# Kernel tuning notes

Hardware: AMD Instinct MI355X
Metric: run time of the kernel (lower is better)

## Reference

```python
import jax, jax.numpy as jnp
import numpy as np

N = 50000      # nodes
E = 400000     # edges (before self loops)
IN = 128       # in_channels
H = 4          # num_heads (layers 1-2)
C = 32         # hidden_dim per head
HID = H * C    # 128 total hidden
CLS = 40       # num_classes (out_heads = 1)
EPS = 1e-5     # BatchNorm eps
SLOPE = 0.2    # LeakyReLU negative slope (PyG GATConv default)


def setup_inputs() -> dict:
    key = jax.random.key(0)
    ks = jax.random.split(key, 24)
    rn = lambda k, shp, s: jax.random.normal(k, shp, jnp.float32) * s
    x = jax.random.normal(ks[0], (N, IN), jnp.float32)
    src = jax.random.randint(ks[1], (E,), 0, N)
    dst = jax.random.randint(ks[2], (E,), 0, N)
    src = jnp.where(src == dst, (src + 1) % N, src)  # no pre-existing self loops
    edge_index = jnp.stack([src, dst]).astype(jnp.int32)
    inp = dict(x=x, edge_index=edge_index)
    # conv1: in IN -> H heads x C
    inp['W1'] = rn(ks[3], (IN, H * C), 1.0 / np.sqrt(IN))
    inp['as1'] = rn(ks[4], (H, C), 0.1)
    inp['ad1'] = rn(ks[5], (H, C), 0.1)
    inp['b1'] = rn(ks[6], (H * C,), 0.02)
    # conv2: HID -> H x C
    inp['W2'] = rn(ks[7], (HID, H * C), 1.0 / np.sqrt(HID))
    inp['as2'] = rn(ks[8], (H, C), 0.1)
    inp['ad2'] = rn(ks[9], (H, C), 0.1)
    inp['b2'] = rn(ks[10], (H * C,), 0.02)
    # conv3: HID -> 1 head x CLS, concat=False
    inp['W3'] = rn(ks[11], (HID, CLS), 1.0 / np.sqrt(HID))
    inp['as3'] = rn(ks[12], (1, CLS), 0.1)
    inp['ad3'] = rn(ks[13], (1, CLS), 0.1)
    inp['b3'] = rn(ks[14], (CLS,), 0.02)
    # residual projection
    inp['Wres'] = rn(ks[15], (IN, HID), 1.0 / np.sqrt(IN))
    # BatchNorm (eval mode: running stats)
    inp['g1'] = 1.0 + rn(ks[16], (HID,), 0.1)
    inp['be1'] = rn(ks[17], (HID,), 0.1)
    inp['m1'] = rn(ks[18], (HID,), 0.1)
    inp['v1'] = 1.0 + jax.random.uniform(ks[19], (HID,), jnp.float32) * 0.5
    inp['g2'] = 1.0 + rn(ks[20], (HID,), 0.1)
    inp['be2'] = rn(ks[21], (HID,), 0.1)
    inp['m2'] = rn(ks[22], (HID,), 0.1)
    inp['v2'] = 1.0 + jax.random.uniform(ks[23], (HID,), jnp.float32) * 0.5
    return inp


def _gat_conv(h, src, dst, W, a_src, a_dst, bias, heads, out_ch, concat):
    """PyG-style GATConv (eval: attention dropout off), self loops already in src/dst."""
    n = h.shape[0]
    xw = (h @ W).reshape(n, heads, out_ch)                    # [N,H,C]
    e_src = jnp.sum(xw * a_src, axis=-1)                      # [N,H]
    e_dst = jnp.sum(xw * a_dst, axis=-1)                      # [N,H]
    e = jax.nn.leaky_relu(e_src[src] + e_dst[dst], SLOPE)     # [E',H]
    # segment softmax over incoming edges of each dst node
    mseg = jax.ops.segment_max(e, dst, num_segments=n)        # [N,H]
    ex = jnp.exp(e - mseg[dst])
    den = jax.ops.segment_sum(ex, dst, num_segments=n)
    alpha = ex / den[dst]                                     # [E',H]
    out = jax.ops.segment_sum(alpha[:, :, None] * xw[src], dst, num_segments=n)  # [N,H,C]
    out = out.reshape(n, heads * out_ch) if concat else out.mean(axis=1)
    return out + bias


def _bn(h, g, b, m, v):
    return (h - m) * jax.lax.rsqrt(v + EPS) * g + b


def reference(x, edge_index, W1, as1, ad1, b1, W2, as2, ad2, b2,
              W3, as3, ad3, b3, Wres, g1, be1, m1, v1, g2, be2, m2, v2):
    n = x.shape[0]
    loop = jnp.arange(n, dtype=edge_index.dtype)
    src = jnp.concatenate([edge_index[0], loop])  # add self loops (PyG default)
    dst = jnp.concatenate([edge_index[1], loop])
    x0 = x
    h = _gat_conv(x0, src, dst, W1, as1, ad1, b1, H, C, True)
    h = jax.nn.elu(_bn(h, g1, be1, m1, v1) + x0 @ Wres)
    h_res = h
    h = _gat_conv(h, src, dst, W2, as2, ad2, b2, H, C, True)
    h = jax.nn.elu(_bn(h, g2, be2, m2, v2) + h_res)
    logits = _gat_conv(h, src, dst, W3, as3, ad3, b3, 1, CLS, False)
    return logits
```

## Files before the change

### kernel.cpp

```cpp
#include <hip/hip_runtime.h>
#include <hip/hip_bf16.h>

#define THREADS 256

typedef __attribute__((ext_vector_type(8))) short bfrag;
typedef __attribute__((ext_vector_type(4))) float f32x4;

__device__ inline unsigned short f2b(float v) {
    __hip_bfloat16 b = __float2bfloat16(v);
    return *reinterpret_cast<unsigned short*>(&b);
}
__device__ inline float b2f(unsigned short u) {
    return __uint_as_float(((unsigned)u) << 16);
}

__global__ void detect_kernel(const unsigned short* __restrict__ x, int n, int* flag) {
    __shared__ int cnt;
    if (threadIdx.x == 0) cnt = 0;
    __syncthreads();
    int local = 0;
    for (int i = threadIdx.x; i < n; i += THREADS) {
        unsigned ex = (x[i] >> 7) & 0xFF;
        if (ex == 0xFF || ex >= 134 || (ex > 0 && ex <= 100)) local++;
    }
    atomicAdd(&cnt, local);
    __syncthreads();
    if (threadIdx.x == 0) *flag = (cnt * 8 > n) ? 0 : 1;
}

struct ConvArgs {
    const void* src[21];
    float* dst[21];
    int prefix[22];
};

__global__ void convert_kernel(ConvArgs a, const int* __restrict__ flag, int total) {
    int i = blockIdx.x * THREADS + threadIdx.x;
    if (i >= total) return;
    bool isbf = (*flag != 0);
    int lo = 0;
    while (i >= a.prefix[lo + 1]) ++lo;
    int off = i - a.prefix[lo];
    float v;
    if (isbf) v = b2f(((const unsigned short*)a.src[lo])[off]);
    else v = ((const float*)a.src[lo])[off];
    a.dst[lo][off] = v;
}

__global__ void xconv_kernel(const float* __restrict__ xin, const int* __restrict__ flag,
                             unsigned short* __restrict__ xb, int total) {
    if (*flag) return;
    int i = blockIdx.x * THREADS + threadIdx.x;
    if (i >= total) return;
    xb[i] = f2b(xin[i]);
}

__global__ void wtf_all(const float* __restrict__ W1, const float* __restrict__ W2,
                        const float* __restrict__ WR, const float* __restrict__ W3,
                        unsigned short* __restrict__ o1, unsigned short* __restrict__ o2,
                        unsigned short* __restrict__ oR, unsigned short* __restrict__ o3) {
    int b = blockIdx.x;
    const float* W; unsigned short* o; int cols, tt;
    if (b < 8)       { W = W1; o = o1; cols = 128; tt = b; }
    else if (b < 16) { W = W2; o = o2; cols = 128; tt = b - 8; }
    else if (b < 24) { W = WR; o = oR; cols = 128; tt = b - 16; }
    else             { W = W3; o = o3; cols = 40;  tt = b - 24; }
    int id = tt * 256 + threadIdx.x;
    int t = id >> 8, ks = (id >> 6) & 3, l = id & 63;
    int q = l >> 4, n = l & 15;
    int c = t * 16 + n;
#pragma unroll
    for (int j = 0; j < 8; ++j) {
        int k = ks * 32 + q * 8 + j;
        float v = (c < cols) ? W[k * cols + c] : 0.f;
        o[id * 8 + j] = f2b(v);
    }
}

__global__ void bnprep_kernel(const float* __restrict__ g1, const float* __restrict__ be1,
                              const float* __restrict__ m1, const float* __restrict__ v1,
                              const float* __restrict__ b1, const float* __restrict__ g2,
                              const float* __restrict__ be2, const float* __restrict__ m2,
                              const float* __restrict__ v2, const float* __restrict__ b2,
                              float* __restrict__ sc1, float* __restrict__ sh1,
                              float* __restrict__ sc2, float* __restrict__ sh2) {
    int c = threadIdx.x;
    if (c < 128) {
        float s = g1[c] * rsqrtf(v1[c] + 1e-5f);
        sc1[c] = s;
        sh1[c] = be1[c] - m1[c] * s + b1[c] * s;
    } else {
        int d = c - 128;
        float s = g2[d] * rsqrtf(v2[d] + 1e-5f);
        sc2[d] = s;
        sh2[d] = be2[d] - m2[d] * s + b2[d] * s;
    }
}

__global__ void count_kernel(const int* __restrict__ ei, int* __restrict__ deg, int E, int N) {
    int e = blockIdx.x * THREADS + threadIdx.x;
    if (e >= E + N) return;
    int d = (e < E) ? ei[E + e] : (e - E);
    atomicAdd(&deg[d], 1);
}

__global__ void bsum_kernel(const int* __restrict__ deg, int* __restrict__ bsum, int N) {
    int idx = blockIdx.x * 256 + threadIdx.x;
    int lane = threadIdx.x & 63, wv = threadIdx.x >> 6;
    int v = (idx < N) ? deg[idx] : 0;
#pragma unroll
    for (int o = 1; o < 64; o <<= 1) v += __shfl_xor(v, o, 64);
    __shared__ int ws[4];
    if (lane == 0) ws[wv] = v;
    __syncthreads();
    if (threadIdx.x == 0) bsum[blockIdx.x] = ws[0] + ws[1] + ws[2] + ws[3];
}

__global__ __launch_bounds__(1024) void bscan_kernel(const int* __restrict__ bsum,
                                                     int* __restrict__ boff, int nb) {
    __shared__ int ws[16];
    int tid = threadIdx.x, lane = tid & 63, wv = tid >> 6;
    int v = (tid < nb) ? bsum[tid] : 0;
    int sc = v;
#pragma unroll
    for (int o = 1; o < 64; o <<= 1) {
        int t = __shfl_up(sc, o, 64);
        if (lane >= o) sc += t;
    }
    if (lane == 63) ws[wv] = sc;
    __syncthreads();
    int add = 0;
#pragma unroll
    for (int k = 0; k < 16; ++k) add += (k < wv) ? ws[k] : 0;
    if (tid < nb) boff[tid] = add + sc - v;
}

__global__ void scanw_kernel(const int* __restrict__ deg, const int* __restrict__ boff,
                             int* __restrict__ row_ptr, int* __restrict__ pos, int N) {
    int idx = blockIdx.x * 256 + threadIdx.x;
    int lane = threadIdx.x & 63, wv = threadIdx.x >> 6;
    int v = (idx < N) ? deg[idx] : 0;
    int sc = v;
#pragma unroll
    for (int o = 1; o < 64; o <<= 1) {
        int t = __shfl_up(sc, o, 64);
        if (lane >= o) sc += t;
    }
    __shared__ int ws[4];
    if (lane == 63) ws[wv] = sc;
    __syncthreads();
    int add = boff[blockIdx.x];
#pragma unroll
    for (int k = 0; k < 4; ++k) add += (k < wv) ? ws[k] : 0;
    int excl = add + sc - v;
    if (idx < N) {
        pos[idx] = excl;
        row_ptr[idx + 1] = excl + v;
    }
    if (idx == 0) row_ptr[0] = 0;
}

__global__ void scatter_kernel(const int* __restrict__ ei, int* __restrict__ pos,
                               int* __restrict__ csr, int E, int N) {
    int e = blockIdx.x * THREADS + threadIdx.x;
    if (e >= E + N) return;
    int s, d;
    if (e < E) { s = ei[e]; d = ei[E + e]; }
    else { s = e - E; d = s; }
    int p = atomicAdd(&pos[d], 1);
    csr[p] = s;
}

template <int COLT, int HEADS, bool ES, typename OT>
__global__ __launch_bounds__(256) void gemm_mfma(
    const unsigned short* __restrict__ A, const unsigned short* __restrict__ Wg,
    const float* __restrict__ as_f, const float* __restrict__ ad_f,
    OT* __restrict__ out, int ldc, int cols,
    float* __restrict__ es, float* __restrict__ ed, int N) {
    __shared__ __align__(16) unsigned short Wls[COLT * 2048];
    int tid = threadIdx.x;
    {
        const float4* src = (const float4*)Wg;
        float4* dst = (float4*)Wls;
#pragma unroll
        for (int i = 0; i < COLT; ++i) dst[tid + i * 256] = src[tid + i * 256];
    }
    __syncthreads();
    int w = tid >> 6, lane = tid & 63;
    int n = lane & 15, q = lane >> 4;
    int row0 = blockIdx.x * 64 + w * 16;
    int ar = row0 + n; ar = ar < N ? ar : N - 1;
    f32x4 acc[COLT];
#pragma unroll
    for (int t = 0; t < COLT; ++t) acc[t] = (f32x4){0.f, 0.f, 0.f, 0.f};
    const unsigned short* arow = A + (size_t)ar * 128;
#pragma unroll
    for (int ks = 0; ks < 4; ++ks) {
        bfrag a = *reinterpret_cast<const bfrag*>(arow + ks * 32 + q * 8);
#pragma unroll
        for (int t = 0; t < COLT; ++t) {
            bfrag b = *reinterpret_cast<const bfrag*>(&Wls[((t * 4 + ks) * 64 + lane) * 8]);
            acc[t] = __builtin_amdgcn_mfma_f32_16x16x32_bf16(a, b, acc[t], 0, 0, 0);
        }
    }
    if (ES) {
        float asv[COLT], adv[COLT];
#pragma unroll
        for (int t = 0; t < COLT; ++t) {
            int c = t * 16 + n;
            asv[t] = (c < cols) ? as_f[c] : 0.f;
            adv[t] = (c < cols) ? ad_f[c] : 0.f;
        }
#pragma unroll
        for (int r = 0; r < 4; ++r) {
            float pe[HEADS], pd[HEADS];
#pragma unroll
            for (int h = 0; h < HEADS; ++h) { pe[h] = 0.f; pd[h] = 0.f; }
#pragma unroll
            for (int t = 0; t < COLT; ++t) {
                int h = (HEADS == 4) ? (t >> 1) : 0;
                pe[h] = fmaf(acc[t][r], asv[t], pe[h]);
                pd[h] = fmaf(acc[t][r], adv[t], pd[h]);
            }
#pragma unroll
            for (int h = 0; h < HEADS; ++h) {
#pragma unroll
                for (int o = 1; o < 16; o <<= 1) {
                    pe[h] += __shfl_xor(pe[h], o, 64);
                    pd[h] += __shfl_xor(pd[h], o, 64);
                }
            }
            int row = row0 + q * 4 + r;
            if (n == 0 && row < N) {
#pragma unroll
                for (int h = 0; h < HEADS; ++h) {
                    es[(size_t)row * HEADS + h] = pe[h];
                    ed[(size_t)row * HEADS + h] = pd[h];
                }
            }
        }
    }
#pragma unroll
    for (int t = 0; t < COLT; ++t) {
        int col = t * 16 + n;
        if (col < cols) {
#pragma unroll
            for (int r = 0; r < 4; ++r) {
                int row = row0 + q * 4 + r;
                if (row < N) {
                    float v = acc[t][r];
                    out[(size_t)row * ldc + col] = (sizeof(OT) == 2) ? (OT)f2b(v) : (OT)v;
                }
            }
        }
    }
}

__global__ __launch_bounds__(256) void gemm_dual(
    const unsigned short* __restrict__ Araw, const unsigned short* __restrict__ Acvt,
    const int* __restrict__ flag,
    const unsigned short* __restrict__ Wg1, const unsigned short* __restrict__ WgR,
    const float* __restrict__ as_f, const float* __restrict__ ad_f,
    unsigned short* __restrict__ xwb, float* __restrict__ resf,
    float* __restrict__ es, float* __restrict__ ed, int N) {
    __shared__ __align__(16) unsigned short Wls[16 * 2048];
    int tid = threadIdx.x;
    {
        const float4* s1 = (const float4*)Wg1;
        const float4* s2 = (const float4*)WgR;
        float4* dst = (float4*)Wls;
#pragma unroll
        for (int i = 0; i < 8; ++i) dst[tid + i * 256] = s1[tid + i * 256];
#pragma unroll
        for (int i = 0; i < 8; ++i) dst[2048 + tid + i * 256] = s2[tid + i * 256];
    }
    const unsigned short* A = (*flag) ? Araw : Acvt;
    __syncthreads();
    int w = tid >> 6, lane = tid & 63;
    int n = lane & 15, q = lane >> 4;
    int row0 = blockIdx.x * 64 + w * 16;
    int ar = row0 + n; ar = ar < N ? ar : N - 1;
    f32x4 acc[16];
#pragma unroll
    for (int t = 0; t < 16; ++t) acc[t] = (f32x4){0.f, 0.f, 0.f, 0.f};
    const unsigned short* arow = A + (size_t)ar * 128;
#pragma unroll
    for (int ks = 0; ks < 4; ++ks) {
        bfrag a = *reinterpret_cast<const bfrag*>(arow + ks * 32 + q * 8);
#pragma unroll
        for (int t = 0; t < 8; ++t) {
            bfrag b = *reinterpret_cast<const bfrag*>(&Wls[((t * 4 + ks) * 64 + lane) * 8]);
            acc[t] = __builtin_amdgcn_mfma_f32_16x16x32_bf16(a, b, acc[t], 0, 0, 0);
        }
#pragma unroll
        for (int t = 0; t < 8; ++t) {
            bfrag b = *reinterpret_cast<const bfrag*>(&Wls[16384 + ((t * 4 + ks) * 64 + lane) * 8]);
            acc[8 + t] = __builtin_amdgcn_mfma_f32_16x16x32_bf16(a, b, acc[8 + t], 0, 0, 0);
        }
    }
    float asv[8], adv[8];
#pragma unroll
    for (int t = 0; t < 8; ++t) {
        int c = t * 16 + n;
        asv[t] = as_f[c];
        adv[t] = ad_f[c];
    }
#pragma unroll
    for (int r = 0; r < 4; ++r) {
        float pe[4] = {0.f, 0.f, 0.f, 0.f}, pd[4] = {0.f, 0.f, 0.f, 0.f};
#pragma unroll
        for (int t = 0; t < 8; ++t) {
            int h = t >> 1;
            pe[h] = fmaf(acc[t][r], asv[t], pe[h]);
            pd[h] = fmaf(acc[t][r], adv[t], pd[h]);
        }
#pragma unroll
        for (int h = 0; h < 4; ++h) {
#pragma unroll
            for (int o = 1; o < 16; o <<= 1) {
                pe[h] += __shfl_xor(pe[h], o, 64);
                pd[h] += __shfl_xor(pd[h], o, 64);
            }
        }
        int row = row0 + q * 4 + r;
        if (n == 0 && row < N) {
#pragma unroll
            for (int h = 0; h < 4; ++h) {
                es[(size_t)row * 4 + h] = pe[h];
                ed[(size_t)row * 4 + h] = pd[h];
            }
        }
    }
#pragma unroll
    for (int t = 0; t < 8; ++t) {
        int col = t * 16 + n;
#pragma unroll
        for (int r = 0; r < 4; ++r) {
            int row = row0 + q * 4 + r;
            if (row < N) {
                xwb[(size_t)row * 128 + col] = f2b(acc[t][r]);
                resf[(size_t)row * 128 + col] = acc[8 + t][r];
            }
        }
    }
}

template <bool WF32>
__global__ __launch_bounds__(256) void agg128_fused(
    const unsigned short* __restrict__ xwb, const float* __restrict__ es,
    const float* __restrict__ ed, const int* __restrict__ row_ptr,
    const int* __restrict__ csr, const float* __restrict__ bnsc,
    const float* __restrict__ bnsh, const float* __restrict__ res,
    float* __restrict__ outf, unsigned short* __restrict__ outb, int N) {
    int w = threadIdx.x >> 6, lane = threadIdx.x & 63;
    int node = blockIdx.x * 4 + w;
    if (node >= N) return;
    int h = lane >> 4;
    int i16 = lane & 15;
    int base = lane & 48;
    int c0 = lane * 2;
    float edl = ed[node * 4 + h];
    int start = row_ptr[node], end = row_ptr[node + 1];
    float den = 0.f, a0 = 0.f, a1 = 0.f;
    for (int jb = start; jb < end; jb += 16) {
        int cnt = end - jb; cnt = cnt < 16 ? cnt : 16;
        int sv = csr[jb + (i16 < cnt ? i16 : 0)];
        float wgl = 0.f;
        if (i16 < cnt) {
            float e = es[sv * 4 + h] + edl;
            e = e > 0.f ? e : 0.2f * e;
            wgl = __expf(e);
        }
        float d = wgl;
        d += __shfl_xor(d, 1, 64);
        d += __shfl_xor(d, 2, 64);
        d += __shfl_xor(d, 4, 64);
        d += __shfl_xor(d, 8, 64);
        den += d;
        for (int j4 = 0; j4 < cnt; j4 += 4) {
#pragma unroll
            for (int u = 0; u < 4; ++u) {
                int j = j4 + u;
                int s = __shfl(sv, j, 64);
                float wg = __shfl(wgl, base + j, 64);
                unsigned uu = *(const unsigned*)(xwb + (size_t)s * 128 + c0);
                a0 = fmaf(wg, __uint_as_float(uu << 16), a0);
                a1 = fmaf(wg, __uint_as_float(uu & 0xffff0000u), a1);
            }
        }
    }
    float inv = 1.f / den;
    float2 sc = *(const float2*)(bnsc + c0);
    float2 sh = *(const float2*)(bnsh + c0);
    float2 rr = *(const float2*)(res + (size_t)node * 128 + c0);
    float v0 = fmaf(a0 * inv, sc.x, sh.x) + rr.x;
    float v1 = fmaf(a1 * inv, sc.y, sh.y) + rr.y;
    v0 = v0 > 0.f ? v0 : expm1f(v0);
    v1 = v1 > 0.f ? v1 : expm1f(v1);
    if (WF32) *(float2*)(outf + (size_t)node * 128 + c0) = make_float2(v0, v1);
    unsigned pk = (unsigned)f2b(v0) | ((unsigned)f2b(v1) << 16);
    *(unsigned*)(outb + (size_t)node * 128 + c0) = pk;
}

__global__ __launch_bounds__(256) void agg40_kernel(
    const unsigned short* __restrict__ xw3b, const float* __restrict__ es3,
    const float* __restrict__ ed3, const int* __restrict__ row_ptr,
    const int* __restrict__ csr, const float* __restrict__ b3,
    void* __restrict__ out, const int* __restrict__ flag, int N) {
    int w = threadIdx.x >> 6, lane = threadIdx.x & 63;
    int node = blockIdx.x * 4 + w;
    if (node >= N) return;
    int i16 = lane & 15;
    int g = lane >= 40 ? 2 : (lane >= 20 ? 1 : 0);
    int cp = lane - g * 20;
    int c0 = cp * 2; c0 = c0 > 38 ? 38 : c0;
    float edl = ed3[node];
    int start = row_ptr[node], end = row_ptr[node + 1];
    float den = 0.f, a0 = 0.f, a1 = 0.f;
    for (int jb = start; jb < end; jb += 16) {
        int cnt = end - jb; cnt = cnt < 16 ? cnt : 16;
        int sv = csr[jb + (i16 < cnt ? i16 : 0)];
        float wgl = 0.f;
        if (i16 < cnt) {
            float e = es3[sv] + edl;
            e = e > 0.f ? e : 0.2f * e;
            wgl = __expf(e);
        }
        float d = wgl;
        d += __shfl_xor(d, 1, 64);
        d += __shfl_xor(d, 2, 64);
        d += __shfl_xor(d, 4, 64);
        d += __shfl_xor(d, 8, 64);
        den += d;
        for (int j = 0; j < cnt; j += 3) {
            int slot = j + g;
            int sl = slot < 15 ? slot : 15;
            int s = __shfl(sv, sl, 64);
            float wg = __shfl(wgl, sl, 64);
            if (slot >= cnt) wg = 0.f;
            unsigned uu = *(const unsigned*)(xw3b + (size_t)s * 40 + c0);
            a0 = fmaf(wg, __uint_as_float(uu << 16), a0);
            a1 = fmaf(wg, __uint_as_float(uu & 0xffff0000u), a1);
        }
    }
    float t0 = __shfl(a0, (lane + 20) & 63, 64);
    float t1 = __shfl(a0, (lane + 40) & 63, 64);
    float u0 = __shfl(a1, (lane + 20) & 63, 64);
    float u1 = __shfl(a1, (lane + 40) & 63, 64);
    a0 += t0 + t1;
    a1 += u0 + u1;
    if (lane < 20) {
        float inv = 1.f / den;
        float v0 = a0 * inv + b3[c0];
        float v1 = a1 * inv + b3[c0 + 1];
        size_t eoff = (size_t)node * 40 + c0;
        if (*flag) {
            unsigned pk = (unsigned)f2b(v0) | ((unsigned)f2b(v1) << 16);
            *(unsigned*)((unsigned short*)out + eoff) = pk;
        } else {
            *(float2*)((float*)out + eoff) = make_float2(v0, v1);
        }
    }
}

extern "C" void kernel_launch(void* const* d_in, const int* in_sizes, int n_in,
                              void* d_out, int out_size, void* d_ws, size_t ws_size,
                              hipStream_t stream) {
    (void)n_in; (void)out_size; (void)ws_size;
    const int N = in_sizes[0] / 128;
    const int E = in_sizes[1] / 2;
    const int EPN = E + N;
    const int NB = (N + 255) / 256;
    char* base = (char*)d_ws;
    size_t off = 0;
    auto alloc = [&](size_t bytes) -> char* {
        char* p = base + off;
        off = (off + bytes + 255) & ~(size_t)255;
        return p;
    };
    int* flag = (int*)alloc(4);
    int* deg = (int*)alloc((size_t)N * 4);
    int* row_ptr = (int*)alloc((size_t)(N + 1) * 4);
    int* pos = (int*)alloc((size_t)N * 4);
    int* bsum = (int*)alloc((size_t)NB * 4);
    int* boff = (int*)alloc((size_t)NB * 4);
    int* csr = (int*)alloc((size_t)EPN * 4);
    float* wc = (float*)alloc((size_t)56184 * 4);
    float* bnsc1 = (float*)alloc(512); float* bnsh1 = (float*)alloc(512);
    float* bnsc2 = (float*)alloc(512); float* bnsh2 = (float*)alloc(512);
    unsigned short* Wl1 = (unsigned short*)alloc(32768);
    unsigned short* Wl2 = (unsigned short*)alloc(32768);
    unsigned short* WlR = (unsigned short*)alloc(32768);
    unsigned short* Wl3 = (unsigned short*)alloc(12288);
    unsigned short* xb = (unsigned short*)alloc((size_t)N * 128 * 2);
    unsigned short* xwb = (unsigned short*)alloc((size_t)N * 128 * 2);
    unsigned short* h1b = (unsigned short*)alloc((size_t)N * 128 * 2);
    float* h1 = (float*)alloc((size_t)N * 128 * 4);
    float* resf = (float*)alloc((size_t)N * 128 * 4);
    float* es = (float*)alloc((size_t)N * 4 * 4);
    float* ed = (float*)alloc((size_t)N * 4 * 4);

    const int* ei = (const int*)d_in[1];

    float* W1 = wc;            float* AS1 = wc + 16384; float* AD1 = wc + 16512; float* B1 = wc + 16640;
    float* W2 = wc + 16768;    float* AS2 = wc + 33152; float* AD2 = wc + 33280; float* B2 = wc + 33408;
    float* W3 = wc + 33536;    float* AS3 = wc + 38656; float* AD3 = wc + 38696; float* B3 = wc + 38736;
    float* WR = wc + 38776;
    float* G1 = wc + 55160; float* BE1 = wc + 55288; float* M1 = wc + 55416; float* V1 = wc + 55544;
    float* G2 = wc + 55672; float* BE2 = wc + 55800; float* M2 = wc + 55928; float* V2 = wc + 56056;

    hipMemsetAsync(deg, 0, (size_t)N * 4, stream);
    detect_kernel<<<1, THREADS, 0, stream>>>((const unsigned short*)d_in[0], 4096, flag);

    ConvArgs ca;
    const int idxs[21] = {2, 3, 4, 5, 6, 7, 8, 9, 10, 11, 12, 13, 14, 15, 16, 17, 18, 19, 20, 21, 22};
    float* dsts[21] = {W1, AS1, AD1, B1, W2, AS2, AD2, B2, W3, AS3, AD3, B3, WR,
                       G1, BE1, M1, V1, G2, BE2, M2, V2};
    int p = 0;
    for (int t = 0; t < 21; t++) {
        ca.src[t] = d_in[idxs[t]];
        ca.dst[t] = dsts[t];
        ca.prefix[t] = p;
        p += in_sizes[idxs[t]];
    }
    ca.prefix[21] = p;
    convert_kernel<<<(p + THREADS - 1) / THREADS, THREADS, 0, stream>>>(ca, flag, p);

    xconv_kernel<<<(N * 128 + THREADS - 1) / THREADS, THREADS, 0, stream>>>(
        (const float*)d_in[0], flag, xb, N * 128);
    wtf_all<<<27, THREADS, 0, stream>>>(W1, W2, WR, W3, Wl1, Wl2, WlR, Wl3);
    bnprep_kernel<<<1, THREADS, 0, stream>>>(G1, BE1, M1, V1, B1, G2, BE2, M2, V2, B2,
                                             bnsc1, bnsh1, bnsc2, bnsh2);

    count_kernel<<<(EPN + THREADS - 1) / THREADS, THREADS, 0, stream>>>(ei, deg, E, N);
    bsum_kernel<<<NB, 256, 0, stream>>>(deg, bsum, N);
    bscan_kernel<<<1, 1024, 0, stream>>>(bsum, boff, NB);
    scanw_kernel<<<NB, 256, 0, stream>>>(deg, boff, row_ptr, pos, N);
    scatter_kernel<<<(EPN + THREADS - 1) / THREADS, THREADS, 0, stream>>>(ei, pos, csr, E, N);

    int gemmGrid = (N + 63) / 64;
    int aggGrid = (N + 3) / 4;

    gemm_dual<<<gemmGrid, 256, 0, stream>>>((const unsigned short*)d_in[0], xb, flag,
                                            Wl1, WlR, AS1, AD1, xwb, resf, es, ed, N);
    agg128_fused<true><<<aggGrid, 256, 0, stream>>>(xwb, es, ed, row_ptr, csr,
                                                    bnsc1, bnsh1, resf, h1, h1b, N);
    gemm_mfma<8, 4, true, unsigned short><<<gemmGrid, 256, 0, stream>>>(
        h1b, Wl2, AS2, AD2, xwb, 128, 128, es, ed, N);
    unsigned short* h2b = (unsigned short*)resf;
    agg128_fused<false><<<aggGrid, 256, 0, stream>>>(xwb, es, ed, row_ptr, csr,
                                                     bnsc2, bnsh2, h1, nullptr, h2b, N);
    gemm_mfma<3, 1, true, unsigned short><<<gemmGrid, 256, 0, stream>>>(
        h2b, Wl3, AS3, AD3, xwb, 40, 40, es, ed, N);
    agg40_kernel<<<aggGrid, 256, 0, stream>>>(xwb, es, ed, row_ptr, csr, B3, d_out, flag, N);
}
```

Measured before the change: 309.1 us.

## Merge prep kernels, store residuals in bf16, and batch gathers in aggregation

Replaces the four separate input-conversion and prep kernels with a single prep kernel that reads raw inputs directly. The residual projection and the layer-1 output now live only in bf16 instead of fp32, which roughly halves that traffic and drops one fp32 write stream. The aggregation loops now issue all 16 neighbor gathers up front, unrolled, to expose memory-level parallelism, at the cost of loading padding rows for partial chunks. The residual path loses precision by going to bf16.

```diff
diff --git a/kernel.cpp b/kernel.cpp
--- a/kernel.cpp
+++ b/kernel.cpp
@@ -12,6 +12,9 @@
 }
 __device__ inline float b2f(unsigned short u) {
     return __uint_as_float(((unsigned)u) << 16);
+}
+__device__ inline float rdv(const void* p, int off, bool isbf) {
+    return isbf ? b2f(((const unsigned short*)p)[off]) : ((const float*)p)[off];
 }
 
 __global__ void detect_kernel(const unsigned short* __restrict__ x, int n, int* flag) {
@@ -28,72 +31,64 @@
     if (threadIdx.x == 0) *flag = (cnt * 8 > n) ? 0 : 1;
 }
 
-struct ConvArgs {
-    const void* src[21];
-    float* dst[21];
-    int prefix[22];
-};
-
-__global__ void convert_kernel(ConvArgs a, const int* __restrict__ flag, int total) {
-    int i = blockIdx.x * THREADS + threadIdx.x;
-    if (i >= total) return;
+struct InPtrs { const void* p[23]; };
+
+__global__ void prep_kernel(InPtrs in, const int* __restrict__ flag,
+                            unsigned short* __restrict__ Wl1, unsigned short* __restrict__ Wl2,
+                            unsigned short* __restrict__ WlR, unsigned short* __restrict__ Wl3,
+                            float* __restrict__ bnsc1, float* __restrict__ bnsh1,
+                            float* __restrict__ bnsc2, float* __restrict__ bnsh2,
+                            float* __restrict__ AS1f, float* __restrict__ AD1f,
+                            float* __restrict__ AS2f, float* __restrict__ AD2f,
+                            float* __restrict__ AS3f, float* __restrict__ AD3f,
+                            float* __restrict__ B3f, unsigned short* __restrict__ xb, int N) {
     bool isbf = (*flag != 0);
-    int lo = 0;
-    while (i >= a.prefix[lo + 1]) ++lo;
-    int off = i - a.prefix[lo];
-    float v;
-    if (isbf) v = b2f(((const unsigned short*)a.src[lo])[off]);
-    else v = ((const float*)a.src[lo])[off];
-    a.dst[lo][off] = v;
-}
-
-__global__ void xconv_kernel(const float* __restrict__ xin, const int* __restrict__ flag,
-                             unsigned short* __restrict__ xb, int total) {
-    if (*flag) return;
-    int i = blockIdx.x * THREADS + threadIdx.x;
-    if (i >= total) return;
-    xb[i] = f2b(xin[i]);
-}
-
-__global__ void wtf_all(const float* __restrict__ W1, const float* __restrict__ W2,
-                        const float* __restrict__ WR, const float* __restrict__ W3,
-                        unsigned short* __restrict__ o1, unsigned short* __restrict__ o2,
-                        unsigned short* __restrict__ oR, unsigned short* __restrict__ o3) {
     int b = blockIdx.x;
-    const float* W; unsigned short* o; int cols, tt;
-    if (b < 8)       { W = W1; o = o1; cols = 128; tt = b; }
-    else if (b < 16) { W = W2; o = o2; cols = 128; tt = b - 8; }
-    else if (b < 24) { W = WR; o = oR; cols = 128; tt = b - 16; }
-    else             { W = W3; o = o3; cols = 40;  tt = b - 24; }
-    int id = tt * 256 + threadIdx.x;
-    int t = id >> 8, ks = (id >> 6) & 3, l = id & 63;
-    int q = l >> 4, n = l & 15;
-    int c = t * 16 + n;
-#pragma unroll
-    for (int j = 0; j < 8; ++j) {
-        int k = ks * 32 + q * 8 + j;
-        float v = (c < cols) ? W[k * cols + c] : 0.f;
-        o[id * 8 + j] = f2b(v);
-    }
-}
-
-__global__ void bnprep_kernel(const float* __restrict__ g1, const float* __restrict__ be1,
-                              const float* __restrict__ m1, const float* __restrict__ v1,
-                              const float* __restrict__ b1, const float* __restrict__ g2,
-                              const float* __restrict__ be2, const float* __restrict__ m2,
-                              const float* __restrict__ v2, const float* __restrict__ b2,
-                              float* __restrict__ sc1, float* __restrict__ sh1,
-                              float* __restrict__ sc2, float* __restrict__ sh2) {
-    int c = threadIdx.x;
-    if (c < 128) {
-        float s = g1[c] * rsqrtf(v1[c] + 1e-5f);
-        sc1[c] = s;
-        sh1[c] = be1[c] - m1[c] * s + b1[c] * s;
+    if (b < 27) {
+        const void* Wv; unsigned short* o; int cols, tt;
+        if (b < 8)       { Wv = in.p[2];  o = Wl1; cols = 128; tt = b; }
+        else if (b < 16) { Wv = in.p[6];  o = Wl2; cols = 128; tt = b - 8; }
+        else if (b < 24) { Wv = in.p[14]; o = WlR; cols = 128; tt = b - 16; }
+        else             { Wv = in.p[10]; o = Wl3; cols = 40;  tt = b - 24; }
+        int id = tt * 256 + threadIdx.x;
+        int t = id >> 8, ks = (id >> 6) & 3, l = id & 63;
+        int q = l >> 4, n = l & 15;
+        int c = t * 16 + n;
+#pragma unroll
+        for (int j = 0; j < 8; ++j) {
+            int k = ks * 32 + q * 8 + j;
+            float v = (c < cols) ? rdv(Wv, k * cols + c, isbf) : 0.f;
+            o[id * 8 + j] = f2b(v);
+        }
+    } else if (b == 27) {
+        int c = threadIdx.x;
+        if (c < 128) {
+            float s = rdv(in.p[15], c, isbf) * rsqrtf(rdv(in.p[18], c, isbf) + 1e-5f);
+            bnsc1[c] = s;
+            bnsh1[c] = rdv(in.p[16], c, isbf) - rdv(in.p[17], c, isbf) * s +
+                       rdv(in.p[5], c, isbf) * s;
+            AS1f[c] = rdv(in.p[3], c, isbf);
+            AD1f[c] = rdv(in.p[4], c, isbf);
+            AS2f[c] = rdv(in.p[7], c, isbf);
+            AD2f[c] = rdv(in.p[8], c, isbf);
+        } else {
+            int d = c - 128;
+            float s = rdv(in.p[19], d, isbf) * rsqrtf(rdv(in.p[22], d, isbf) + 1e-5f);
+            bnsc2[d] = s;
+            bnsh2[d] = rdv(in.p[20], d, isbf) - rdv(in.p[21], d, isbf) * s +
+                       rdv(in.p[9], d, isbf) * s;
+            if (d < 40) {
+                AS3f[d] = rdv(in.p[11], d, isbf);
+                AD3f[d] = rdv(in.p[12], d, isbf);
+                B3f[d] = rdv(in.p[13], d, isbf);
+            }
+        }
     } else {
-        int d = c - 128;
-        float s = g2[d] * rsqrtf(v2[d] + 1e-5f);
-        sc2[d] = s;
-        sh2[d] = be2[d] - m2[d] * s + b2[d] * s;
+        if (isbf) return;
+        const float* xf = (const float*)in.p[0];
+        int total = N * 128;
+        int stride = (gridDim.x - 28) * 256;
+        for (int i = (b - 28) * 256 + threadIdx.x; i < total; i += stride) xb[i] = f2b(xf[i]);
     }
 }
 
@@ -171,11 +166,11 @@
     csr[p] = s;
 }
 
-template <int COLT, int HEADS, bool ES, typename OT>
+template <int COLT, int HEADS, bool ES>
 __global__ __launch_bounds__(256) void gemm_mfma(
     const unsigned short* __restrict__ A, const unsigned short* __restrict__ Wg,
     const float* __restrict__ as_f, const float* __restrict__ ad_f,
-    OT* __restrict__ out, int ldc, int cols,
+    unsigned short* __restrict__ out, int ldc, int cols,
     float* __restrict__ es, float* __restrict__ ed, int N) {
     __shared__ __align__(16) unsigned short Wls[COLT * 2048];
     int tid = threadIdx.x;
@@ -247,10 +242,7 @@
 #pragma unroll
             for (int r = 0; r < 4; ++r) {
                 int row = row0 + q * 4 + r;
-                if (row < N) {
-                    float v = acc[t][r];
-                    out[(size_t)row * ldc + col] = (sizeof(OT) == 2) ? (OT)f2b(v) : (OT)v;
-                }
+                if (row < N) out[(size_t)row * ldc + col] = f2b(acc[t][r]);
             }
         }
     }
@@ -261,7 +253,7 @@
     const int* __restrict__ flag,
     const unsigned short* __restrict__ Wg1, const unsigned short* __restrict__ WgR,
     const float* __restrict__ as_f, const float* __restrict__ ad_f,
-    unsigned short* __restrict__ xwb, float* __restrict__ resf,
+    unsigned short* __restrict__ xwb, unsigned short* __restrict__ resb,
     float* __restrict__ es, float* __restrict__ ed, int N) {
     __shared__ __align__(16) unsigned short Wls[16 * 2048];
     int tid = threadIdx.x;
@@ -339,19 +331,18 @@
             int row = row0 + q * 4 + r;
             if (row < N) {
                 xwb[(size_t)row * 128 + col] = f2b(acc[t][r]);
-                resf[(size_t)row * 128 + col] = acc[8 + t][r];
-            }
-        }
-    }
-}
-
-template <bool WF32>
+                resb[(size_t)row * 128 + col] = f2b(acc[8 + t][r]);
+            }
+        }
+    }
+}
+
 __global__ __launch_bounds__(256) void agg128_fused(
     const unsigned short* __restrict__ xwb, const float* __restrict__ es,
     const float* __restrict__ ed, const int* __restrict__ row_ptr,
     const int* __restrict__ csr, const float* __restrict__ bnsc,
-    const float* __restrict__ bnsh, const float* __restrict__ res,
-    float* __restrict__ outf, unsigned short* __restrict__ outb, int N) {
+    const float* __restrict__ bnsh, const unsigned short* __restrict__ resb,
+    unsigned short* __restrict__ outb, int N) {
     int w = threadIdx.x >> 6, lane = threadIdx.x & 63;
     int node = blockIdx.x * 4 + w;
     if (node >= N) return;
@@ -365,6 +356,12 @@
     for (int jb = start; jb < end; jb += 16) {
         int cnt = end - jb; cnt = cnt < 16 ? cnt : 16;
         int sv = csr[jb + (i16 < cnt ? i16 : 0)];
+        unsigned uu[16];
+#pragma unroll
+        for (int u = 0; u < 16; ++u) {
+            int s = __shfl(sv, u, 64);
+            uu[u] = *(const unsigned*)(xwb + (size_t)s * 128 + c0);
+        }
         float wgl = 0.f;
         if (i16 < cnt) {
             float e = es[sv * 4 + h] + edl;
@@ -377,27 +374,21 @@
         d += __shfl_xor(d, 4, 64);
         d += __shfl_xor(d, 8, 64);
         den += d;
-        for (int j4 = 0; j4 < cnt; j4 += 4) {
-#pragma unroll
-            for (int u = 0; u < 4; ++u) {
-                int j = j4 + u;
-                int s = __shfl(sv, j, 64);
-                float wg = __shfl(wgl, base + j, 64);
-                unsigned uu = *(const unsigned*)(xwb + (size_t)s * 128 + c0);
-                a0 = fmaf(wg, __uint_as_float(uu << 16), a0);
-                a1 = fmaf(wg, __uint_as_float(uu & 0xffff0000u), a1);
-            }
+#pragma unroll
+        for (int u = 0; u < 16; ++u) {
+            float wg = __shfl(wgl, base + u, 64);
+            a0 = fmaf(wg, __uint_as_float(uu[u] << 16), a0);
+            a1 = fmaf(wg, __uint_as_float(uu[u] & 0xffff0000u), a1);
         }
     }
     float inv = 1.f / den;
     float2 sc = *(const float2*)(bnsc + c0);
     float2 sh = *(const float2*)(bnsh + c0);
-    float2 rr = *(const float2*)(res + (size_t)node * 128 + c0);
-    float v0 = fmaf(a0 * inv, sc.x, sh.x) + rr.x;
-    float v1 = fmaf(a1 * inv, sc.y, sh.y) + rr.y;
+    unsigned ur = *(const unsigned*)(resb + (size_t)node * 128 + c0);
+    float v0 = fmaf(a0 * inv, sc.x, sh.x) + __uint_as_float(ur << 16);
+    float v1 = fmaf(a1 * inv, sc.y, sh.y) + __uint_as_float(ur & 0xffff0000u);
     v0 = v0 > 0.f ? v0 : expm1f(v0);
     v1 = v1 > 0.f ? v1 : expm1f(v1);
-    if (WF32) *(float2*)(outf + (size_t)node * 128 + c0) = make_float2(v0, v1);
     unsigned pk = (unsigned)f2b(v0) | ((unsigned)f2b(v1) << 16);
     *(unsigned*)(outb + (size_t)node * 128 + c0) = pk;
 }
@@ -420,6 +411,13 @@
     for (int jb = start; jb < end; jb += 16) {
         int cnt = end - jb; cnt = cnt < 16 ? cnt : 16;
         int sv = csr[jb + (i16 < cnt ? i16 : 0)];
+        unsigned uu[6];
+#pragma unroll
+        for (int t = 0; t < 6; ++t) {
+            int slot = 3 * t + g; slot = slot < 15 ? slot : 15;
+            int s = __shfl(sv, slot, 64);
+            uu[t] = *(const unsigned*)(xw3b + (size_t)s * 40 + c0);
+        }
         float wgl = 0.f;
         if (i16 < cnt) {
             float e = es3[sv] + edl;
@@ -432,15 +430,14 @@
         d += __shfl_xor(d, 4, 64);
         d += __shfl_xor(d, 8, 64);
         den += d;
-        for (int j = 0; j < cnt; j += 3) {
-            int slot = j + g;
+#pragma unroll
+        for (int t = 0; t < 6; ++t) {
+            int slot = 3 * t + g;
             int sl = slot < 15 ? slot : 15;
-            int s = __shfl(sv, sl, 64);
             float wg = __shfl(wgl, sl, 64);
             if (slot >= cnt) wg = 0.f;
-            unsigned uu = *(const unsigned*)(xw3b + (size_t)s * 40 + c0);
-            a0 = fmaf(wg, __uint_as_float(uu << 16), a0);
-            a1 = fmaf(wg, __uint_as_float(uu & 0xffff0000u), a1);
+            a0 = fmaf(wg, __uint_as_float(uu[t] << 16), a0);
+            a1 = fmaf(wg, __uint_as_float(uu[t] & 0xffff0000u), a1);
         }
     }
     float t0 = __shfl(a0, (lane + 20) & 63, 64);
@@ -485,9 +482,12 @@
     int* bsum = (int*)alloc((size_t)NB * 4);
     int* boff = (int*)alloc((size_t)NB * 4);
     int* csr = (int*)alloc((size_t)EPN * 4);
-    float* wc = (float*)alloc((size_t)56184 * 4);
     float* bnsc1 = (float*)alloc(512); float* bnsh1 = (float*)alloc(512);
     float* bnsc2 = (float*)alloc(512); float* bnsh2 = (float*)alloc(512);
+    float* AS1f = (float*)alloc(512); float* AD1f = (float*)alloc(512);
+    float* AS2f = (float*)alloc(512); float* AD2f = (float*)alloc(512);
+    float* AS3f = (float*)alloc(256); float* AD3f = (float*)alloc(256);
+    float* B3f = (float*)alloc(256);
     unsigned short* Wl1 = (unsigned short*)alloc(32768);
     unsigned short* Wl2 = (unsigned short*)alloc(32768);
     unsigned short* WlR = (unsigned short*)alloc(32768);
@@ -495,42 +495,21 @@
     unsigned short* xb = (unsigned short*)alloc((size_t)N * 128 * 2);
     unsigned short* xwb = (unsigned short*)alloc((size_t)N * 128 * 2);
     unsigned short* h1b = (unsigned short*)alloc((size_t)N * 128 * 2);
-    float* h1 = (float*)alloc((size_t)N * 128 * 4);
-    float* resf = (float*)alloc((size_t)N * 128 * 4);
+    unsigned short* resb = (unsigned short*)alloc((size_t)N * 128 * 2);
     float* es = (float*)alloc((size_t)N * 4 * 4);
     float* ed = (float*)alloc((size_t)N * 4 * 4);
 
     const int* ei = (const int*)d_in[1];
 
-    float* W1 = wc;            float* AS1 = wc + 16384; float* AD1 = wc + 16512; float* B1 = wc + 16640;
-    float* W2 = wc + 16768;    float* AS2 = wc + 33152; float* AD2 = wc + 33280; float* B2 = wc + 33408;
-    float* W3 = wc + 33536;    float* AS3 = wc + 38656; float* AD3 = wc + 38696; float* B3 = wc + 38736;
-    float* WR = wc + 38776;
-    float* G1 = wc + 55160; float* BE1 = wc + 55288; float* M1 = wc + 55416; float* V1 = wc + 55544;
-    float* G2 = wc + 55672; float* BE2 = wc + 55800; float* M2 = wc + 55928; float* V2 = wc + 56056;
-
     hipMemsetAsync(deg, 0, (size_t)N * 4, stream);
     detect_kernel<<<1, THREADS, 0, stream>>>((const unsigned short*)d_in[0], 4096, flag);
 
-    ConvArgs ca;
-    const int idxs[21] = {2, 3, 4, 5, 6, 7, 8, 9, 10, 11, 12, 13, 14, 15, 16, 17, 18, 19, 20, 21, 22};
-    float* dsts[21] = {W1, AS1, AD1, B1, W2, AS2, AD2, B2, W3, AS3, AD3, B3, WR,
-                       G1, BE1, M1, V1, G2, BE2, M2, V2};
-    int p = 0;
-    for (int t = 0; t < 21; t++) {
-        ca.src[t] = d_in[idxs[t]];
-        ca.dst[t] = dsts[t];
-        ca.prefix[t] = p;
-        p += in_sizes[idxs[t]];
-    }
-    ca.prefix[21] = p;
-    convert_kernel<<<(p + THREADS - 1) / THREADS, THREADS, 0, stream>>>(ca, flag, p);
-
-    xconv_kernel<<<(N * 128 + THREADS - 1) / THREADS, THREADS, 0, stream>>>(
-        (const float*)d_in[0], flag, xb, N * 128);
-    wtf_all<<<27, THREADS, 0, stream>>>(W1, W2, WR, W3, Wl1, Wl2, WlR, Wl3);
-    bnprep_kernel<<<1, THREADS, 0, stream>>>(G1, BE1, M1, V1, B1, G2, BE2, M2, V2, B2,
-                                             bnsc1, bnsh1, bnsc2, bnsh2);
+    InPtrs ip;
+    for (int t = 0; t < 23; t++) ip.p[t] = d_in[t];
+    prep_kernel<<<28 + 2048, THREADS, 0, stream>>>(ip, flag, Wl1, Wl2, WlR, Wl3,
+                                                   bnsc1, bnsh1, bnsc2, bnsh2,
+                                                   AS1f, AD1f, AS2f, AD2f,
+                                                   AS3f, AD3f, B3f, xb, N);
 
     count_kernel<<<(EPN + THREADS - 1) / THREADS, THREADS, 0, stream>>>(ei, deg, E, N);
     bsum_kernel<<<NB, 256, 0, stream>>>(deg, bsum, N);
@@ -542,15 +521,15 @@
     int aggGrid = (N + 3) / 4;
 
     gemm_dual<<<gemmGrid, 256, 0, stream>>>((const unsigned short*)d_in[0], xb, flag,
-                                            Wl1, WlR, AS1, AD1, xwb, resf, es, ed, N);
-    agg128_fused<true><<<aggGrid, 256, 0, stream>>>(xwb, es, ed, row_ptr, csr,
-                                                    bnsc1, bnsh1, resf, h1, h1b, N);
-    gemm_mfma<8, 4, true, unsigned short><<<gemmGrid, 256, 0, stream>>>(
-        h1b, Wl2, AS2, AD2, xwb, 128, 128, es, ed, N);
-    unsigned short* h2b = (unsigned short*)resf;
-    agg128_fused<false><<<aggGrid, 256, 0, stream>>>(xwb, es, ed, row_ptr, csr,
-                                                     bnsc2, bnsh2, h1, nullptr, h2b, N);
-    gemm_mfma<3, 1, true, unsigned short><<<gemmGrid, 256, 0, stream>>>(
-        h2b, Wl3, AS3, AD3, xwb, 40, 40, es, ed, N);
-    agg40_kernel<<<aggGrid, 256, 0, stream>>>(xwb, es, ed, row_ptr, csr, B3, d_out, flag, N);
-}
+                                            Wl1, WlR, AS1f, AD1f, xwb, resb, es, ed, N);
+    agg128_fused<<<aggGrid, 256, 0, stream>>>(xwb, es, ed, row_ptr, csr,
+                                              bnsc1, bnsh1, resb, h1b, N);
+    gemm_mfma<8, 4, true><<<gemmGrid, 256, 0, stream>>>(
+        h1b, Wl2, AS2f, AD2f, xwb, 128, 128, es, ed, N);
+    unsigned short* h2b = resb;
+    agg128_fused<<<aggGrid, 256, 0, stream>>>(xwb, es, ed, row_ptr, csr,
+                                              bnsc2, bnsh2, h1b, h2b, N);
+    gemm_mfma<3, 1, true><<<gemmGrid, 256, 0, stream>>>(
+        h2b, Wl3, AS3f, AD3f, xwb, 40, 40, es, ed, N);
+    agg40_kernel<<<aggGrid, 256, 0, stream>>>(xwb, es, ed, row_ptr, csr, B3f, d_out, flag, N);
+}
```

Result: faster. 300.6 us (-2.7%).
